# Optimization experiments

Measured on AMD Instinct MI355X. Metric: run time of the kernel, lower is better.

The kernel has to match this reference:

```python
import jax, jax.numpy as jnp
import numpy as np
import math

B, Q, CQ = 2, 2048, 512
H, D = 8, 64  # no_heads, c_hidden

def setup_inputs() -> dict:
    key = jax.random.key(0)
    ks = jax.random.split(key, 8)
    s = 0.02
    return {
        "q_x": jax.random.normal(ks[0], (B, Q, CQ), jnp.float32),
        "kv_x": jax.random.normal(ks[1], (B, Q, CQ), jnp.float32),
        "bias": jax.random.normal(ks[2], (B, 1, Q, Q), jnp.float32),
        "w_qkv": jax.random.normal(ks[3], (3 * H * D, CQ), jnp.float32) * s,
        "w_o": jax.random.normal(ks[4], (CQ, H * D), jnp.float32) * s,
        "b_o": jnp.zeros((CQ,), jnp.float32),
        "w_g": jax.random.normal(ks[5], (H * D, CQ), jnp.float32) * s,
        "b_g": jnp.zeros((H * D,), jnp.float32),
    }

def reference(q_x, kv_x, bias, w_qkv, w_o, b_o, w_g, b_g):
    # Fused QKV projection from q_x (kv_x is unused by the original module's _prep_qkv)
    qkv = jnp.einsum('bqc,ec->bqe', q_x, w_qkv)  # [B,Q,3*H*D]
    q, k, v = jnp.split(qkv, 3, axis=-1)
    q = q.reshape(B, Q, H, D) / math.sqrt(D)
    k = k.reshape(B, Q, H, D)
    v = v.reshape(B, Q, H, D)
    # scores + additive pairwise bias, softmax over keys
    scores = jnp.einsum('bqhd,bkhd->bhqk', q, k) + bias  # [B,H,Q,K]
    attn = jax.nn.softmax(scores, axis=-1)
    o = jnp.einsum('bhqk,bkhd->bqhd', attn, v)  # [B,Q,H,D]
    # sigmoid gating
    g = jax.nn.sigmoid(jnp.einsum('bqc,ec->bqe', q_x, w_g) + b_g).reshape(B, Q, H, D)
    o = o * g
    # output projection
    o = o.reshape(B, Q, H * D)
    return jnp.einsum('bqe,ce->bqc', o, w_o) + b_o
```

## Files before the change

### kernel.cpp

```cpp
#include <hip/hip_runtime.h>
#include <math.h>

#define B_  2
#define Q_  2048
#define CQ_ 512
#define H_  8
#define D_  64
#define M_  (B_*Q_)
#define L2E 1.44269504088896f

typedef __bf16 bf16;
typedef __bf16 bf16x4 __attribute__((ext_vector_type(4)));
typedef __bf16 bf16x8 __attribute__((ext_vector_type(8)));
typedef float  f32x4  __attribute__((ext_vector_type(4)));
typedef float  f32x16 __attribute__((ext_vector_type(16)));

__device__ __forceinline__ void gl_lds16(const bf16* g, bf16* l) {
    __builtin_amdgcn_global_load_lds(
        (const __attribute__((address_space(1))) unsigned int*)g,
        (__attribute__((address_space(3))) unsigned int*)l, 16, 0, 0);
}

#define S0 (4096*512)
#define S1 (1536*512)
#define S2 (512*512)
#define S3 (512*512)
__global__ __launch_bounds__(256)
void convert_kernel(const float* __restrict__ qx, const float* __restrict__ wqkv,
                    const float* __restrict__ wg, const float* __restrict__ wo,
                    bf16* __restrict__ qxb, bf16* __restrict__ wcat, bf16* __restrict__ wob)
{
    const long long t = (long long)blockIdx.x * 256 + threadIdx.x;
    const long long e = t * 8;
    const float* src; bf16* dst;
    if (e < S0)                { src = qx + e;                  dst = qxb + e; }
    else if (e < S0 + S1)      { src = wqkv + (e - S0);         dst = wcat + (e - S0); }
    else if (e < S0 + S1 + S2) { src = wg + (e - S0 - S1);      dst = wcat + S1 + (e - S0 - S1); }
    else                       { src = wo + (e - S0 - S1 - S2); dst = wob + (e - S0 - S1 - S2); }
    const float4 a = *(const float4*)(src);
    const float4 b = *(const float4*)(src + 4);
    bf16x8 v;
    v[0] = (bf16)a.x; v[1] = (bf16)a.y; v[2] = (bf16)a.z; v[3] = (bf16)a.w;
    v[4] = (bf16)b.x; v[5] = (bf16)b.y; v[6] = (bf16)b.z; v[7] = (bf16)b.w;
    *(bf16x8*)dst = v;
}

template<int BM, int BN, int EPI>
__global__ __launch_bounds__(256)
void gemm_bf16(const bf16* __restrict__ A, const bf16* __restrict__ W,
               const float* __restrict__ bvec, float* __restrict__ fout,
               bf16* __restrict__ qb, bf16* __restrict__ kb, bf16* __restrict__ vb,
               bf16* __restrict__ gb)
{
    constexpr int MI = BM / 32, NJ = BN / 32;
    __shared__ __align__(16) bf16 As[BM * 32];
    __shared__ __align__(16) bf16 Bs[BN * 32];

    const int t = threadIdx.x;
    const int w = t >> 6, lane = t & 63;
    const int l15 = lane & 15, quad = lane >> 4;
    const int wm = w & 1, wn = w >> 1;
    const int bm = blockIdx.x * BM;
    const int bn = blockIdx.y * BN;
    const bool swapped = (EPI == 1) || ((bn >> 9) != 2);

    f32x4 acc[MI][NJ] = {};

    const int rr = t >> 2;
    const int cc = (t & 3) * 8;

    for (int k0 = 0; k0 < 512; k0 += 32) {
        #pragma unroll
        for (int i = 0; i < BM / 64; ++i)
            gl_lds16(A + (size_t)(bm + i * 64 + rr) * 512 + k0 + cc,
                     As + (i * 64 + w * 16) * 32);
        #pragma unroll
        for (int i = 0; i < BN / 64; ++i)
            gl_lds16(W + (size_t)(bn + i * 64 + rr) * 512 + k0 + cc,
                     Bs + (i * 64 + w * 16) * 32);
        __asm__ volatile("s_waitcnt vmcnt(0)" ::: "memory");
        __syncthreads();

        bf16x8 af[MI], bfr[NJ];
        #pragma unroll
        for (int i = 0; i < MI; ++i)
            af[i] = *(const bf16x8*)(As + (wm * (BM / 2) + i * 16 + l15) * 32 + quad * 8);
        #pragma unroll
        for (int j = 0; j < NJ; ++j)
            bfr[j] = *(const bf16x8*)(Bs + (wn * (BN / 2) + j * 16 + l15) * 32 + quad * 8);
        if (swapped) {
            #pragma unroll
            for (int i = 0; i < MI; ++i)
                #pragma unroll
                for (int j = 0; j < NJ; ++j)
                    acc[i][j] = __builtin_amdgcn_mfma_f32_16x16x32_bf16(bfr[j], af[i], acc[i][j], 0, 0, 0);
        } else {
            #pragma unroll
            for (int i = 0; i < MI; ++i)
                #pragma unroll
                for (int j = 0; j < NJ; ++j)
                    acc[i][j] = __builtin_amdgcn_mfma_f32_16x16x32_bf16(af[i], bfr[j], acc[i][j], 0, 0, 0);
        }
        __syncthreads();
    }

    if (swapped) {
        #pragma unroll
        for (int i = 0; i < MI; ++i) {
            const int m = bm + wm * (BM / 2) + i * 16 + l15;
            const int b = m >> 11, qq = m & 2047;
            #pragma unroll
            for (int j = 0; j < NJ; ++j) {
                const int n0 = bn + wn * (BN / 2) + j * 16 + quad * 4;
                const f32x4 cv = acc[i][j];
                if constexpr (EPI == 1) {
                    float4 st;
                    st.x = cv[0] + bvec[n0 + 0];
                    st.y = cv[1] + bvec[n0 + 1];
                    st.z = cv[2] + bvec[n0 + 2];
                    st.w = cv[3] + bvec[n0 + 3];
                    *(float4*)(fout + (size_t)m * 512 + n0) = st;
                } else {
                    const int part = n0 >> 9;
                    if (part == 0) {
                        const int h = (n0 >> 6) & 7, d0 = n0 & 63;
                        bf16x4 q4;
                        #pragma unroll
                        for (int r = 0; r < 4; ++r) q4[r] = (bf16)(cv[r] * (0.125f * L2E));
                        *(bf16x4*)(qb + (size_t)(b * H_ + h) * (Q_ * D_) + (size_t)qq * 64 + d0) = q4;
                    } else if (part == 1) {
                        const int h = (n0 >> 6) & 7, d0 = n0 & 63;
                        const size_t off = (size_t)(b * H_ + h) * (Q_ * D_)
                            + (qq >> 6) * 4096 + ((qq >> 5) & 1) * 2048
                            + (d0 >> 4) * 512 + ((d0 >> 3) & 1) * 256
                            + (qq & 31) * 8 + (d0 & 7);
                        bf16x4 k4;
                        #pragma unroll
                        for (int r = 0; r < 4; ++r) k4[r] = (bf16)cv[r];
                        *(bf16x4*)(kb + off) = k4;
                    } else {
                        const int gcol = n0 & 511;
                        const float4 bv4 = *(const float4*)(bvec + gcol);
                        bf16x4 g4;
                        g4[0] = (bf16)(1.f / (1.f + __expf(-(cv[0] + bv4.x))));
                        g4[1] = (bf16)(1.f / (1.f + __expf(-(cv[1] + bv4.y))));
                        g4[2] = (bf16)(1.f / (1.f + __expf(-(cv[2] + bv4.z))));
                        g4[3] = (bf16)(1.f / (1.f + __expf(-(cv[3] + bv4.w))));
                        *(bf16x4*)(gb + (size_t)m * 512 + gcol) = g4;
                    }
                }
            }
        }
    } else {
        #pragma unroll
        for (int i = 0; i < MI; ++i) {
            const int m0 = bm + wm * (BM / 2) + i * 16 + quad * 4;
            const int b = m0 >> 11, qq0 = m0 & 2047;
            #pragma unroll
            for (int j = 0; j < NJ; ++j) {
                const int n = bn + wn * (BN / 2) + j * 16 + l15;
                const int h = (n >> 6) & 7, d = n & 63;
                const size_t off = (size_t)(b * H_ + h) * (Q_ * D_)
                    + (qq0 >> 6) * 4096 + (d >> 5) * 2048
                    + ((qq0 & 63) >> 4) * 512 + ((qq0 >> 3) & 1) * 256
                    + (d & 31) * 8 + (qq0 & 7);
                bf16x4 v4;
                #pragma unroll
                for (int r = 0; r < 4; ++r) v4[r] = (bf16)acc[i][j][r];
                *(bf16x4*)(vb + off) = v4;
            }
        }
    }
}

__global__ __launch_bounds__(256, 3)
void attn_part(const bf16* __restrict__ qb, const bf16* __restrict__ kf,
               const bf16* __restrict__ vf, const float* __restrict__ bias,
               bf16* __restrict__ po, float2* __restrict__ ml)
{
    __shared__ __align__(16) bf16 Ks[2][4096];
    __shared__ __align__(16) bf16 Vs[2][4096];
    __shared__ __align__(16) bf16 Ps[4][32 * 72];

    const int tid  = threadIdx.x;
    const int wv   = tid >> 6, lane = tid & 63;
    const int l31  = lane & 31, b5 = lane >> 5;
    const int x    = blockIdx.x;
    const int bh   = ((x & 7) << 1) | (x >> 3);
    const int b    = bh >> 3;
    const int qg   = blockIdx.y * 128 + wv * 32 + l31;
    const int ks   = blockIdx.z;

    const bf16* qp = qb + ((size_t)bh * Q_ + qg) * D_;
    bf16x8 bq[4];
    #pragma unroll
    for (int c = 0; c < 4; ++c)
        bq[c] = *(const bf16x8*)(qp + c * 16 + b5 * 8);

    f32x16 acc[2] = {};
    float m_run = -INFINITY, l_run = 0.f;

    const bf16*  kfb  = kf + (size_t)bh * (Q_ * D_) + (size_t)ks * 16 * 4096;
    const bf16*  vfb  = vf + (size_t)bh * (Q_ * D_) + (size_t)ks * 16 * 4096;
    const float* brow = bias + ((size_t)b * Q_ + qg) * Q_ + ks * 1024;

    f32x4 bcur[8], bnxt[8];

    #pragma unroll
    for (int p = 0; p < 2; ++p) {
        gl_lds16(kfb + (wv * 2 + p) * 512 + lane * 8, Ks[0] + (wv * 2 + p) * 512);
        gl_lds16(vfb + (wv * 2 + p) * 512 + lane * 8, Vs[0] + (wv * 2 + p) * 512);
    }
    #pragma unroll
    for (int i = 0; i < 8; ++i)
        bcur[i] = *(const f32x4*)(brow + (i >> 2) * 32 + (i & 3) * 8 + b5 * 4);
    __asm__ volatile("s_waitcnt vmcnt(0)" ::: "memory");
    __syncthreads();

    bf16* pw = Ps[wv] + l31 * 72;

    int cur = 0;
    #pragma unroll 1
    for (int t = 0; t < 16; ++t) {
        if (t < 15) {
            const size_t off = (size_t)(t + 1) * 4096;
            #pragma unroll
            for (int p = 0; p < 2; ++p) {
                gl_lds16(kfb + off + (wv * 2 + p) * 512 + lane * 8,
                         Ks[cur ^ 1] + (wv * 2 + p) * 512);
                gl_lds16(vfb + off + (wv * 2 + p) * 512 + lane * 8,
                         Vs[cur ^ 1] + (wv * 2 + p) * 512);
            }
            const int k0n = (t + 1) * 64;
            #pragma unroll
            for (int i = 0; i < 8; ++i)
                bnxt[i] = *(const f32x4*)(brow + k0n + (i >> 2) * 32 + (i & 3) * 8 + b5 * 4);
        }

        const bf16* Kc = Ks[cur];
        f32x16 sv[2] = {};
        #pragma unroll
        for (int kg = 0; kg < 2; ++kg)
            #pragma unroll
            for (int c = 0; c < 4; ++c) {
                const bf16x8 ak = *(const bf16x8*)(Kc + kg * 2048 + c * 512 + lane * 8);
                sv[kg] = __builtin_amdgcn_mfma_f32_32x32x16_bf16(ak, bq[c], sv[kg], 0, 0, 0);
            }

        float sc[2][16];
        #pragma unroll
        for (int kg = 0; kg < 2; ++kg)
            #pragma unroll
            for (int r = 0; r < 16; ++r)
                sc[kg][r] = fmaf(bcur[kg * 4 + (r >> 2)][r & 3], L2E, sv[kg][r]);

        float tmax = -INFINITY;
        #pragma unroll
        for (int kg = 0; kg < 2; ++kg)
            #pragma unroll
            for (int r = 0; r < 16; ++r)
                tmax = fmaxf(tmax, sc[kg][r]);
        tmax = fmaxf(tmax, __shfl_xor(tmax, 32, 64));

        const float mn = fmaxf(m_run, tmax);
        const float alpha = __builtin_amdgcn_exp2f(m_run - mn);
        m_run = mn;

        float rsum = 0.f;
        #pragma unroll
        for (int kg = 0; kg < 2; ++kg)
            #pragma unroll
            for (int r = 0; r < 16; ++r) {
                sc[kg][r] = __builtin_amdgcn_exp2f(sc[kg][r] - mn);
                rsum += sc[kg][r];
            }
        rsum += __shfl_xor(rsum, 32, 64);
        l_run = l_run * alpha + rsum;
        acc[0] *= alpha;
        acc[1] *= alpha;

        #pragma unroll
        for (int kg = 0; kg < 2; ++kg)
            #pragma unroll
            for (int gi = 0; gi < 4; ++gi) {
                bf16x4 p4;
                p4[0] = (bf16)sc[kg][gi * 4 + 0];
                p4[1] = (bf16)sc[kg][gi * 4 + 1];
                p4[2] = (bf16)sc[kg][gi * 4 + 2];
                p4[3] = (bf16)sc[kg][gi * 4 + 3];
                *(bf16x4*)(pw + kg * 32 + gi * 8 + b5 * 4) = p4;
            }
        __asm__ volatile("s_waitcnt lgkmcnt(0)" ::: "memory");

        const bf16* Vc = Vs[cur];
        #pragma unroll
        for (int c4 = 0; c4 < 4; ++c4) {
            const bf16x8 bp = *(const bf16x8*)(pw + c4 * 16 + b5 * 8);
            #pragma unroll
            for (int dg = 0; dg < 2; ++dg) {
                const bf16x8 av = *(const bf16x8*)(Vc + dg * 2048 + c4 * 512 + lane * 8);
                acc[dg] = __builtin_amdgcn_mfma_f32_32x32x16_bf16(av, bp, acc[dg], 0, 0, 0);
            }
        }

        if (t < 15) {
            #pragma unroll
            for (int i = 0; i < 8; ++i) bcur[i] = bnxt[i];
        }
        __asm__ volatile("s_waitcnt vmcnt(0)" ::: "memory");
        __syncthreads();
        cur ^= 1;
    }

    const float inv = 1.f / l_run;
    const size_t pbase = ((size_t)(ks * 16 + bh) * Q_ + qg) * 64;
    #pragma unroll
    for (int dg = 0; dg < 2; ++dg)
        #pragma unroll
        for (int gi = 0; gi < 4; ++gi) {
            const int d0 = dg * 32 + gi * 8 + b5 * 4;
            bf16x4 ov;
            #pragma unroll
            for (int r = 0; r < 4; ++r)
                ov[r] = (bf16)(acc[dg][gi * 4 + r] * inv);
            *(bf16x4*)(po + pbase + d0) = ov;
        }
    if (b5 == 0)
        ml[(size_t)(ks * 16 + bh) * Q_ + qg] = make_float2(m_run, l_run);
}

__global__ __launch_bounds__(256)
void merge_kernel(const bf16* __restrict__ po, const float2* __restrict__ ml,
                  const bf16* __restrict__ g, bf16* __restrict__ og)
{
    const int gid = blockIdx.x * 256 + threadIdx.x;
    const int row = gid >> 3;
    const int d8  = (gid & 7) * 8;
    const int bh  = row >> 11, qg = row & 2047;
    const int b   = bh >> 3, h = bh & 7;

    const float2 ml0 = ml[row];
    const float2 ml1 = ml[16 * Q_ + row];
    const float  M   = fmaxf(ml0.x, ml1.x);
    const float  w0r = ml0.y * __builtin_amdgcn_exp2f(ml0.x - M);
    const float  w1r = ml1.y * __builtin_amdgcn_exp2f(ml1.x - M);
    const float  inv = 1.f / (w0r + w1r);
    const float  w0 = w0r * inv, w1 = w1r * inv;

    const bf16x8 o0 = *(const bf16x8*)(po + (size_t)row * 64 + d8);
    const bf16x8 o1 = *(const bf16x8*)(po + (size_t)16 * Q_ * 64 + (size_t)row * 64 + d8);
    const size_t obase = ((size_t)(b * Q_ + qg)) * 512 + h * 64 + d8;
    const bf16x8 gv = *(const bf16x8*)(g + obase);
    bf16x8 ov;
    #pragma unroll
    for (int r = 0; r < 8; ++r)
        ov[r] = (bf16)(((float)o0[r] * w0 + (float)o1[r] * w1) * (float)gv[r]);
    *(bf16x8*)(og + obase) = ov;
}

extern "C" void kernel_launch(void* const* d_in, const int* in_sizes, int n_in,
                              void* d_out, int out_size, void* d_ws, size_t ws_size,
                              hipStream_t stream)
{
    const float* q_x   = (const float*)d_in[0];
    const float* bias  = (const float*)d_in[2];
    const float* w_qkv = (const float*)d_in[3];
    const float* w_o   = (const float*)d_in[4];
    const float* b_o   = (const float*)d_in[5];
    const float* w_g   = (const float*)d_in[6];
    const float* b_g   = (const float*)d_in[7];
    float* out = (float*)d_out;

    char* ws = (char*)d_ws;
    bf16*   qxb  = (bf16*)(ws);
    bf16*   wcat = (bf16*)(ws + (4u  << 20));
    bf16*   po   = (bf16*)(ws);
    bf16*   qb   = (bf16*)(ws + (8u  << 20));
    bf16*   kb   = (bf16*)(ws + (12u << 20));
    bf16*   vb   = (bf16*)(ws + (16u << 20));
    bf16*   gb   = (bf16*)(ws + (20u << 20));
    bf16*   ogb  = (bf16*)(ws + (24u << 20));
    bf16*   wob  = (bf16*)(ws + (28u << 20));
    float2* ml   = (float2*)(ws + (28u << 20) + (1u << 19));

    convert_kernel<<<(S0 + S1 + S2 + S3) / (256 * 8), 256, 0, stream>>>(
        q_x, w_qkv, w_g, w_o, qxb, wcat, wob);
    gemm_bf16<128, 128, 0><<<dim3(32, 16), 256, 0, stream>>>(
        qxb, wcat, b_g, nullptr, qb, kb, vb, gb);
    attn_part<<<dim3(B_ * H_, Q_ / 128, 2), 256, 0, stream>>>(qb, kb, vb, bias, po, ml);
    merge_kernel<<<(16 * Q_ * 8) / 256, 256, 0, stream>>>(po, ml, gb, ogb);
    gemm_bf16<64, 128, 1><<<dim3(64, 4), 256, 0, stream>>>(
        ogb, wob, b_o, out, nullptr, nullptr, nullptr, nullptr);
}
```

Measured before the change: 179.8 us.

## Split attention keys four ways and pass P in registers via permlane swap

```diff
diff --git a/kernel.cpp b/kernel.cpp
--- a/kernel.cpp
+++ b/kernel.cpp
@@ -14,11 +14,18 @@
 typedef __bf16 bf16x8 __attribute__((ext_vector_type(8)));
 typedef float  f32x4  __attribute__((ext_vector_type(4)));
 typedef float  f32x16 __attribute__((ext_vector_type(16)));
+typedef unsigned int u32x2 __attribute__((ext_vector_type(2)));
 
 __device__ __forceinline__ void gl_lds16(const bf16* g, bf16* l) {
     __builtin_amdgcn_global_load_lds(
         (const __attribute__((address_space(1))) unsigned int*)g,
         (__attribute__((address_space(3))) unsigned int*)l, 16, 0, 0);
+}
+
+__device__ __forceinline__ unsigned int cvtpk_bf16(float lo, float hi) {
+    unsigned int r;
+    asm("v_cvt_pk_bf16_f32 %0, %1, %2" : "=v"(r) : "v"(lo), "v"(hi));
+    return r;
 }
 
 #define S0 (4096*512)
@@ -173,14 +180,13 @@
     }
 }
 
-__global__ __launch_bounds__(256, 3)
+__global__ __launch_bounds__(256, 4)
 void attn_part(const bf16* __restrict__ qb, const bf16* __restrict__ kf,
                const bf16* __restrict__ vf, const float* __restrict__ bias,
                bf16* __restrict__ po, float2* __restrict__ ml)
 {
     __shared__ __align__(16) bf16 Ks[2][4096];
     __shared__ __align__(16) bf16 Vs[2][4096];
-    __shared__ __align__(16) bf16 Ps[4][32 * 72];
 
     const int tid  = threadIdx.x;
     const int wv   = tid >> 6, lane = tid & 63;
@@ -200,9 +206,9 @@
     f32x16 acc[2] = {};
     float m_run = -INFINITY, l_run = 0.f;
 
-    const bf16*  kfb  = kf + (size_t)bh * (Q_ * D_) + (size_t)ks * 16 * 4096;
-    const bf16*  vfb  = vf + (size_t)bh * (Q_ * D_) + (size_t)ks * 16 * 4096;
-    const float* brow = bias + ((size_t)b * Q_ + qg) * Q_ + ks * 1024;
+    const bf16*  kfb  = kf + (size_t)bh * (Q_ * D_) + (size_t)ks * 8 * 4096;
+    const bf16*  vfb  = vf + (size_t)bh * (Q_ * D_) + (size_t)ks * 8 * 4096;
+    const float* brow = bias + ((size_t)b * Q_ + qg) * Q_ + ks * 512;
 
     f32x4 bcur[8], bnxt[8];
 
@@ -217,12 +223,10 @@
     __asm__ volatile("s_waitcnt vmcnt(0)" ::: "memory");
     __syncthreads();
 
-    bf16* pw = Ps[wv] + l31 * 72;
-
     int cur = 0;
     #pragma unroll 1
-    for (int t = 0; t < 16; ++t) {
-        if (t < 15) {
+    for (int t = 0; t < 8; ++t) {
+        if (t < 7) {
             const size_t off = (size_t)(t + 1) * 4096;
             #pragma unroll
             for (int p = 0; p < 2; ++p) {
@@ -239,6 +243,7 @@
 
         const bf16* Kc = Ks[cur];
         f32x16 sv[2] = {};
+        __builtin_amdgcn_s_setprio(1);
         #pragma unroll
         for (int kg = 0; kg < 2; ++kg)
             #pragma unroll
@@ -246,6 +251,7 @@
                 const bf16x8 ak = *(const bf16x8*)(Kc + kg * 2048 + c * 512 + lane * 8);
                 sv[kg] = __builtin_amdgcn_mfma_f32_32x32x16_bf16(ak, bq[c], sv[kg], 0, 0, 0);
             }
+        __builtin_amdgcn_s_setprio(0);
 
         float sc[2][16];
         #pragma unroll
@@ -254,56 +260,68 @@
             for (int r = 0; r < 16; ++r)
                 sc[kg][r] = fmaf(bcur[kg * 4 + (r >> 2)][r & 3], L2E, sv[kg][r]);
 
-        float tmax = -INFINITY;
-        #pragma unroll
-        for (int kg = 0; kg < 2; ++kg)
-            #pragma unroll
-            for (int r = 0; r < 16; ++r)
-                tmax = fmaxf(tmax, sc[kg][r]);
+        float mx[16];
+        #pragma unroll
+        for (int r = 0; r < 16; ++r) mx[r] = fmaxf(sc[0][r], sc[1][r]);
+        #pragma unroll
+        for (int r = 0; r < 8; ++r) mx[r] = fmaxf(mx[r], mx[r + 8]);
+        #pragma unroll
+        for (int r = 0; r < 4; ++r) mx[r] = fmaxf(mx[r], mx[r + 4]);
+        float tmax = fmaxf(fmaxf(mx[0], mx[1]), fmaxf(mx[2], mx[3]));
         tmax = fmaxf(tmax, __shfl_xor(tmax, 32, 64));
 
         const float mn = fmaxf(m_run, tmax);
         const float alpha = __builtin_amdgcn_exp2f(m_run - mn);
         m_run = mn;
 
-        float rsum = 0.f;
         #pragma unroll
         for (int kg = 0; kg < 2; ++kg)
             #pragma unroll
-            for (int r = 0; r < 16; ++r) {
+            for (int r = 0; r < 16; ++r)
                 sc[kg][r] = __builtin_amdgcn_exp2f(sc[kg][r] - mn);
-                rsum += sc[kg][r];
-            }
+
+        float sm[16];
+        #pragma unroll
+        for (int r = 0; r < 16; ++r) sm[r] = sc[0][r] + sc[1][r];
+        #pragma unroll
+        for (int r = 0; r < 8; ++r) sm[r] += sm[r + 8];
+        #pragma unroll
+        for (int r = 0; r < 4; ++r) sm[r] += sm[r + 4];
+        float rsum = (sm[0] + sm[1]) + (sm[2] + sm[3]);
         rsum += __shfl_xor(rsum, 32, 64);
         l_run = l_run * alpha + rsum;
         acc[0] *= alpha;
         acc[1] *= alpha;
 
+        bf16x8 bp[4];
         #pragma unroll
         for (int kg = 0; kg < 2; ++kg)
             #pragma unroll
-            for (int gi = 0; gi < 4; ++gi) {
-                bf16x4 p4;
-                p4[0] = (bf16)sc[kg][gi * 4 + 0];
-                p4[1] = (bf16)sc[kg][gi * 4 + 1];
-                p4[2] = (bf16)sc[kg][gi * 4 + 2];
-                p4[3] = (bf16)sc[kg][gi * 4 + 3];
-                *(bf16x4*)(pw + kg * 32 + gi * 8 + b5 * 4) = p4;
-            }
-        __asm__ volatile("s_waitcnt lgkmcnt(0)" ::: "memory");
+            for (int h = 0; h < 2; ++h) {
+                const unsigned int u  = cvtpk_bf16(sc[kg][8 * h + 0], sc[kg][8 * h + 1]);
+                const unsigned int u2 = cvtpk_bf16(sc[kg][8 * h + 2], sc[kg][8 * h + 3]);
+                const unsigned int vv = cvtpk_bf16(sc[kg][8 * h + 4], sc[kg][8 * h + 5]);
+                const unsigned int v2 = cvtpk_bf16(sc[kg][8 * h + 6], sc[kg][8 * h + 7]);
+                const u32x2 s1 = __builtin_amdgcn_permlane32_swap(u,  vv, false, false);
+                const u32x2 s2 = __builtin_amdgcn_permlane32_swap(u2, v2, false, false);
+                union { unsigned int w[4]; bf16x8 v8; } pkw;
+                pkw.w[0] = s1[0]; pkw.w[1] = s2[0]; pkw.w[2] = s1[1]; pkw.w[3] = s2[1];
+                bp[kg * 2 + h] = pkw.v8;
+            }
 
         const bf16* Vc = Vs[cur];
+        __builtin_amdgcn_s_setprio(1);
         #pragma unroll
         for (int c4 = 0; c4 < 4; ++c4) {
-            const bf16x8 bp = *(const bf16x8*)(pw + c4 * 16 + b5 * 8);
             #pragma unroll
             for (int dg = 0; dg < 2; ++dg) {
                 const bf16x8 av = *(const bf16x8*)(Vc + dg * 2048 + c4 * 512 + lane * 8);
-                acc[dg] = __builtin_amdgcn_mfma_f32_32x32x16_bf16(av, bp, acc[dg], 0, 0, 0);
-            }
-        }
-
-        if (t < 15) {
+                acc[dg] = __builtin_amdgcn_mfma_f32_32x32x16_bf16(av, bp[c4], acc[dg], 0, 0, 0);
+            }
+        }
+        __builtin_amdgcn_s_setprio(0);
+
+        if (t < 7) {
             #pragma unroll
             for (int i = 0; i < 8; ++i) bcur[i] = bnxt[i];
         }
@@ -339,22 +357,35 @@
     const int bh  = row >> 11, qg = row & 2047;
     const int b   = bh >> 3, h = bh & 7;
 
-    const float2 ml0 = ml[row];
-    const float2 ml1 = ml[16 * Q_ + row];
-    const float  M   = fmaxf(ml0.x, ml1.x);
-    const float  w0r = ml0.y * __builtin_amdgcn_exp2f(ml0.x - M);
-    const float  w1r = ml1.y * __builtin_amdgcn_exp2f(ml1.x - M);
-    const float  inv = 1.f / (w0r + w1r);
-    const float  w0 = w0r * inv, w1 = w1r * inv;
-
-    const bf16x8 o0 = *(const bf16x8*)(po + (size_t)row * 64 + d8);
-    const bf16x8 o1 = *(const bf16x8*)(po + (size_t)16 * Q_ * 64 + (size_t)row * 64 + d8);
+    float2 m4[4];
+    #pragma unroll
+    for (int s = 0; s < 4; ++s) m4[s] = ml[(size_t)s * (16 * Q_) + row];
+    const float M = fmaxf(fmaxf(m4[0].x, m4[1].x), fmaxf(m4[2].x, m4[3].x));
+    float w[4], tot = 0.f;
+    #pragma unroll
+    for (int s = 0; s < 4; ++s) {
+        w[s] = m4[s].y * __builtin_amdgcn_exp2f(m4[s].x - M);
+        tot += w[s];
+    }
+    const float inv = 1.f / tot;
+    #pragma unroll
+    for (int s = 0; s < 4; ++s) w[s] *= inv;
+
+    bf16x8 o[4];
+    #pragma unroll
+    for (int s = 0; s < 4; ++s)
+        o[s] = *(const bf16x8*)(po + (size_t)s * (16 * Q_ * 64) + (size_t)row * 64 + d8);
+
     const size_t obase = ((size_t)(b * Q_ + qg)) * 512 + h * 64 + d8;
     const bf16x8 gv = *(const bf16x8*)(g + obase);
     bf16x8 ov;
     #pragma unroll
-    for (int r = 0; r < 8; ++r)
-        ov[r] = (bf16)(((float)o0[r] * w0 + (float)o1[r] * w1) * (float)gv[r]);
+    for (int r = 0; r < 8; ++r) {
+        float acc = 0.f;
+        #pragma unroll
+        for (int s = 0; s < 4; ++s) acc += (float)o[s][r] * w[s];
+        ov[r] = (bf16)(acc * (float)gv[r]);
+    }
     *(bf16x8*)(og + obase) = ov;
 }
 
@@ -375,19 +406,19 @@
     bf16*   qxb  = (bf16*)(ws);
     bf16*   wcat = (bf16*)(ws + (4u  << 20));
     bf16*   po   = (bf16*)(ws);
-    bf16*   qb   = (bf16*)(ws + (8u  << 20));
-    bf16*   kb   = (bf16*)(ws + (12u << 20));
-    bf16*   vb   = (bf16*)(ws + (16u << 20));
-    bf16*   gb   = (bf16*)(ws + (20u << 20));
-    bf16*   ogb  = (bf16*)(ws + (24u << 20));
-    bf16*   wob  = (bf16*)(ws + (28u << 20));
-    float2* ml   = (float2*)(ws + (28u << 20) + (1u << 19));
+    bf16*   qb   = (bf16*)(ws + (16u << 20));
+    bf16*   kb   = (bf16*)(ws + (20u << 20));
+    bf16*   vb   = (bf16*)(ws + (24u << 20));
+    bf16*   gb   = (bf16*)(ws + (28u << 20));
+    bf16*   ogb  = (bf16*)(ws + (32u << 20));
+    bf16*   wob  = (bf16*)(ws + (36u << 20));
+    float2* ml   = (float2*)(ws + (36u << 20) + (1u << 19));
 
     convert_kernel<<<(S0 + S1 + S2 + S3) / (256 * 8), 256, 0, stream>>>(
         q_x, w_qkv, w_g, w_o, qxb, wcat, wob);
     gemm_bf16<128, 128, 0><<<dim3(32, 16), 256, 0, stream>>>(
         qxb, wcat, b_g, nullptr, qb, kb, vb, gb);
-    attn_part<<<dim3(B_ * H_, Q_ / 128, 2), 256, 0, stream>>>(qb, kb, vb, bias, po, ml);
+    attn_part<<<dim3(B_ * H_, Q_ / 128, 4), 256, 0, stream>>>(qb, kb, vb, bias, po, ml);
     merge_kernel<<<(16 * Q_ * 8) / 256, 256, 0, stream>>>(po, ml, gb, ogb);
     gemm_bf16<64, 128, 1><<<dim3(64, 4), 256, 0, stream>>>(
         ogb, wob, b_o, out, nullptr, nullptr, nullptr, nullptr);
```

Result: slower. 276.6 us (+53.8%).
